# Kernel optimization log

Hardware: AMD Instinct MI355X
Metric: run time of the kernel (lower is better)

## Reference

```python
import jax, jax.numpy as jnp
import numpy as np

COUNT = 8  # hardcoded 8x8 patch grid in the original module


def setup_inputs() -> dict:
    key = jax.random.key(0)
    kx, = jax.random.split(key, 1)
    x = jax.random.normal(kx, (8, 64, 512, 512), dtype=jnp.float32)
    gamma = jnp.zeros((1,), dtype=jnp.float32)  # nn.Parameter(torch.zeros(1))
    return {"x": x, "gamma": gamma}


def reference(x, gamma):
    B, C, H, W = x.shape
    s = H // COUNT  # stride; original uses height-derived stride for both dims
    # Extract the 8x8 grid of patches without loops:
    # (B,C,H,W) -> (B,C,cnt,s,cnt,s) -> (B,cnt,cnt,C,s,s) -> (B,P,C,s*s)
    p = x.reshape(B, C, COUNT, s, COUNT, s)
    p = p.transpose(0, 2, 4, 1, 3, 5).reshape(B, COUNT * COUNT, C, s * s)
    # channel-channel energy per patch: [B,P,C,C]
    energy = jnp.einsum('bpci,bpdi->bpcd', p, p)
    # DANet trick: max - energy, then softmax over last dim
    energy_new = jnp.max(energy, axis=-1, keepdims=True) - energy
    attention = jax.nn.softmax(energy_new, axis=-1)
    out = jnp.einsum('bpcd,bpdi->bpci', attention, p)
    # reassemble spatial map
    out = out.reshape(B, COUNT, COUNT, C, s, s)
    out = out.transpose(0, 3, 1, 4, 2, 5).reshape(B, C, H, W)
    # NOTE: in the torch code y = x is an alias and x is overwritten in-place,
    # so the final result is gamma * attended + attended.
    return gamma[0] * out + out
```

## Files before the change

### kernel.cpp

```cpp
#include <hip/hip_runtime.h>


#define NC  64
#define NW  512
#define HWs 262144
#define NST 32

typedef __attribute__((ext_vector_type(8)))  __bf16 bf8;
typedef __attribute__((ext_vector_type(16))) float  f32x16;

__device__ __forceinline__ unsigned short bf16rne(float f) {
  unsigned int u = __float_as_uint(f);
  u += 0x7fffu + ((u >> 16) & 1u);
  return (unsigned short)(u >> 16);
}
__device__ __forceinline__ float fromb(unsigned short h) {
  return __uint_as_float(((unsigned int)h) << 16);
}

extern "C" __global__ __launch_bounds__(256, 4)
void spectralAgg_kernel(const float* __restrict__ x, const float* __restrict__ g,
                        float* __restrict__ out) {
  __shared__ char lds[40960];
  char* sH = lds;
  char* sL = lds + 16384;
  char* sA = lds + 32768;

  const int t   = threadIdx.x;
  const int wv  = t >> 6;
  const int l   = t & 63;
  const int l31 = l & 31;
  const int hh  = l >> 5;

  const int wg = blockIdx.x;
  const int b  = wg >> 6;
  const int pp = wg & 63;
  const int pr = pp >> 3, pc = pp & 7;
  const size_t pbase = (size_t)b * NC * HWs + (size_t)(pr * 64) * NW + (size_t)(pc * 64);
  const float* xp = x + pbase;
  float* op = out + pbase;

  const int ct = wv >> 1, dt = wv & 1;
  f32x16 accG, accS;
#pragma unroll
  for (int r = 0; r < 16; ++r) { accG[r] = 0.f; accS[r] = 0.f; }

  const char* pA  = sH + (ct * 32 + l31) * 256;
  const char* pBh = sH + (dt * 32 + l31) * 256;
  const char* pBl = sL + (dt * 32 + l31) * 256;
  const int swzH = (l & 15) << 4;

  for (int st = 0; st < NST; ++st) {
#pragma unroll 4
    for (int k = 0; k < 8; ++k) {
      const int L = t + (k << 8);
      const int c = L >> 5, q = L & 31;
      const int rl = q >> 4, col = (q & 15) << 2;
      const float4 v = *(const float4*)(xp + (size_t)c * HWs + (size_t)(st * 2 + rl) * NW + col);
      const int i0  = rl * 64 + col;
      const int off = (c << 8) + (((i0 << 1)) ^ ((c & 15) << 4));
      const unsigned short h0 = bf16rne(v.x), h1 = bf16rne(v.y),
                           h2 = bf16rne(v.z), h3 = bf16rne(v.w);
      ushort4 hv; hv.x = h0; hv.y = h1; hv.z = h2; hv.w = h3;
      *(ushort4*)(sH + off) = hv;
      ushort4 lv;
      lv.x = bf16rne(v.x - fromb(h0));
      lv.y = bf16rne(v.y - fromb(h1));
      lv.z = bf16rne(v.z - fromb(h2));
      lv.w = bf16rne(v.w - fromb(h3));
      *(ushort4*)(sL + off) = lv;
    }
    __syncthreads();
#pragma unroll
    for (int k0 = 0; k0 < 8; ++k0) {
      const int off = ((k0 << 5) + (hh << 4)) ^ swzH;
      const bf8 a  = *(const bf8*)(pA  + off);
      const bf8 bh = *(const bf8*)(pBh + off);
      const bf8 bl = *(const bf8*)(pBl + off);
      accG = __builtin_amdgcn_mfma_f32_32x32x16_bf16(a, bh, accG, 0, 0, 0);
      accS = __builtin_amdgcn_mfma_f32_32x32x16_bf16(a, bl, accS, 0, 0, 0);
    }
    __syncthreads();
  }

  float* S_lds = (float*)sL;
  float* E_lds = (float*)sH;
#pragma unroll
  for (int r = 0; r < 16; ++r) {
    const int cr = ct * 32 + (r & 3) + ((r >> 2) << 3) + (hh << 2);
    S_lds[cr * 64 + dt * 32 + l31] = accS[r];
  }
  __syncthreads();
#pragma unroll
  for (int r = 0; r < 16; ++r) {
    const int cr = ct * 32 + (r & 3) + ((r >> 2) << 3) + (hh << 2);
    const int d  = dt * 32 + l31;
    E_lds[cr * 64 + d] = accG[r] + accS[r] + S_lds[d * 64 + cr];
  }
  __syncthreads();

  const float gs = 1.0f + g[0];
#pragma unroll 1
  for (int rr = 0; rr < 16; ++rr) {
    const int c = wv * 16 + rr;
    const float e = E_lds[c * 64 + l];
    float mn = e;
#pragma unroll
    for (int o = 32; o; o >>= 1) mn = fminf(mn, __shfl_xor(mn, o));
    const float w = __expf(mn - e);
    float s = w;
#pragma unroll
    for (int o = 32; o; o >>= 1) s += __shfl_xor(s, o);
    const float a = gs * w / s;
    *(unsigned short*)(sA + c * 128 + (((l << 1)) ^ ((c & 7) << 4))) = bf16rne(a);
  }
  __syncthreads();

  char* sT = sH;
  const int irow = wv * 32 + l31;
  const char* pP  = sT + irow * 128;
  const int swzT  = (((irow & 7) ^ ((irow >> 3) & 3)) << 4);
  const char* pA0 = sA + l31 * 128;
  const char* pA1 = sA + (32 + l31) * 128;
  const int swzA  = (l31 & 7) << 4;

  for (int st = 0; st < NST; ++st) {
#pragma unroll 2
    for (int k = 0; k < 2; ++k) {
      const int L = t + (k << 8);
      const int cg = L >> 5, q = L & 31;
      const int c0 = cg << 2;
      const int rl = q >> 4, col = (q & 15) << 2;
      const int i0 = rl * 64 + col;
      const float* gp = xp + (size_t)c0 * HWs + (size_t)(st * 2 + rl) * NW + col;
      const float4 v0 = *(const float4*)(gp);
      const float4 v1 = *(const float4*)(gp + HWs);
      const float4 v2 = *(const float4*)(gp + 2 * (size_t)HWs);
      const float4 v3 = *(const float4*)(gp + 3 * (size_t)HWs);
      float vv[4][4];
      vv[0][0] = v0.x; vv[0][1] = v0.y; vv[0][2] = v0.z; vv[0][3] = v0.w;
      vv[1][0] = v1.x; vv[1][1] = v1.y; vv[1][2] = v1.z; vv[1][3] = v1.w;
      vv[2][0] = v2.x; vv[2][1] = v2.y; vv[2][2] = v2.z; vv[2][3] = v2.w;
      vv[3][0] = v3.x; vv[3][1] = v3.y; vv[3][2] = v3.z; vv[3][3] = v3.w;
#pragma unroll
      for (int ii = 0; ii < 4; ++ii) {
        const int ir = i0 + ii;
        ushort4 wq;
        wq.x = bf16rne(vv[0][ii]); wq.y = bf16rne(vv[1][ii]);
        wq.z = bf16rne(vv[2][ii]); wq.w = bf16rne(vv[3][ii]);
        *(ushort4*)(sT + ir * 128 + (((c0 << 1)) ^ ((((ir & 7) ^ ((ir >> 3) & 3))) << 4))) = wq;
      }
    }
    __syncthreads();

    f32x16 o0, o1;
#pragma unroll
    for (int r = 0; r < 16; ++r) { o0[r] = 0.f; o1[r] = 0.f; }
#pragma unroll
    for (int k0 = 0; k0 < 4; ++k0) {
      const int km = (k0 << 5) + (hh << 4);
      const bf8 pa = *(const bf8*)(pP  + (km ^ swzT));
      const bf8 a0 = *(const bf8*)(pA0 + (km ^ swzA));
      const bf8 a1 = *(const bf8*)(pA1 + (km ^ swzA));
      o0 = __builtin_amdgcn_mfma_f32_32x32x16_bf16(pa, a0, o0, 0, 0, 0);
      o1 = __builtin_amdgcn_mfma_f32_32x32x16_bf16(pa, a1, o1, 0, 0, 0);
    }

#pragma unroll
    for (int rq = 0; rq < 4; ++rq) {
      const int iloc = wv * 32 + (rq << 3) + (hh << 2);
      const int grow = st * 2 + (iloc >> 6), gcol = iloc & 63;
      float* oprow = op + (size_t)grow * NW + gcol;
      float4 q0; q0.x = o0[rq * 4 + 0]; q0.y = o0[rq * 4 + 1];
                 q0.z = o0[rq * 4 + 2]; q0.w = o0[rq * 4 + 3];
      *(float4*)(oprow + (size_t)l31 * HWs) = q0;
      float4 q1; q1.x = o1[rq * 4 + 0]; q1.y = o1[rq * 4 + 1];
                 q1.z = o1[rq * 4 + 2]; q1.w = o1[rq * 4 + 3];
      *(float4*)(oprow + (size_t)(32 + l31) * HWs) = q1;
    }
    __syncthreads();
  }
}

extern "C" void kernel_launch(void* const* d_in, const int* in_sizes, int n_in,
                              void* d_out, int out_size, void* d_ws, size_t ws_size,
                              hipStream_t stream) {
  const float* x = (const float*)d_in[0];
  const float* g = (const float*)d_in[1];
  float* o = (float*)d_out;
  spectralAgg_kernel<<<dim3(512), dim3(256), 0, stream>>>(x, g, o);
}
```

Baseline: 439.4 us.

## Register-prefetch next tile and double stage width in both GEMM phases

Both phases now process four rows per stage instead of two, which halves the number of stage iterations and barriers. Each stage's global loads are prefetched into registers one step ahead so load latency overlaps the MFMA work. The attention B-fragments are hoisted into registers once before the output loop, and hardware bf16 conversions replace the manual rounding code. LDS grows to 72KB and occupancy drops to 2 blocks per CU, with much higher register pressure from the 32 float4 prefetch buffers.

```diff
diff --git a/kernel.cpp b/kernel.cpp
--- a/kernel.cpp
+++ b/kernel.cpp
@@ -1,30 +1,75 @@
 #include <hip/hip_runtime.h>
 
 
-#define NC  64
 #define NW  512
 #define HWs 262144
-#define NST 32
+#define NS1 16
+#define NS3 16
 
 typedef __attribute__((ext_vector_type(8)))  __bf16 bf8;
+typedef __attribute__((ext_vector_type(4)))  __bf16 bf4;
 typedef __attribute__((ext_vector_type(16))) float  f32x16;
 
-__device__ __forceinline__ unsigned short bf16rne(float f) {
-  unsigned int u = __float_as_uint(f);
-  u += 0x7fffu + ((u >> 16) & 1u);
-  return (unsigned short)(u >> 16);
-}
-__device__ __forceinline__ float fromb(unsigned short h) {
-  return __uint_as_float(((unsigned int)h) << 16);
-}
-
-extern "C" __global__ __launch_bounds__(256, 4)
+#define F4C(v, k) ((k) == 0 ? (v).x : (k) == 1 ? (v).y : (k) == 2 ? (v).z : (v).w)
+
+__device__ __forceinline__ void load1(const float* g1, int st, float4 (&R)[16]) {
+  const float* gp = g1 + (size_t)st * 4 * NW;
+#pragma unroll
+  for (int rl = 0; rl < 4; ++rl)
+#pragma unroll
+    for (int j = 0; j < 4; ++j)
+      R[rl * 4 + j] = *(const float4*)(gp + (size_t)rl * NW + j * 4);
+}
+
+__device__ __forceinline__ void cvtw1(char* wH, char* wL, int q_ld, int swzw,
+                                      const float4 (&R)[16]) {
+#pragma unroll
+  for (int rl = 0; rl < 4; ++rl)
+#pragma unroll
+    for (int s = 0; s < 2; ++s) {
+      const float4 va = R[rl * 4 + s * 2], vb = R[rl * 4 + s * 2 + 1];
+      const float f[8] = {va.x, va.y, va.z, va.w, vb.x, vb.y, vb.z, vb.w};
+      bf8 h, lo;
+#pragma unroll
+      for (int e = 0; e < 8; ++e) {
+        h[e]  = (__bf16)f[e];
+        lo[e] = (__bf16)(f[e] - (float)h[e]);
+      }
+      const int boff = (rl * 128 + q_ld * 32 + s * 16) ^ swzw;
+      *(bf8*)(wH + boff) = h;
+      *(bf8*)(wL + boff) = lo;
+    }
+}
+
+__device__ __forceinline__ void load3(const float* g3, int st, float4 (&R)[16]) {
+  const float* gp = g3 + (size_t)st * 4 * NW;
+#pragma unroll
+  for (int cc = 0; cc < 4; ++cc)
+#pragma unroll
+    for (int j = 0; j < 4; ++j)
+      R[cc * 4 + j] = *(const float4*)(gp + (size_t)cc * HWs + j * 4);
+}
+
+__device__ __forceinline__ void cvtw3(char* sT, int cg, int iq, const float4 (&R)[16]) {
+#pragma unroll
+  for (int w = 0; w < 16; ++w) {
+    bf4 q;
+#pragma unroll
+    for (int cc = 0; cc < 4; ++cc)
+      q[cc] = (__bf16)F4C(R[cc * 4 + (w >> 2)], w & 3);
+    const int iloc = iq * 16 + w;
+    const int boff = (iloc & 127) * 256 + (((((iloc >> 7) << 7)) + cg * 8) ^ (w << 4));
+    *(bf4*)(sT + boff) = q;
+  }
+}
+
+extern "C" __global__ __launch_bounds__(256, 2)
 void spectralAgg_kernel(const float* __restrict__ x, const float* __restrict__ g,
                         float* __restrict__ out) {
-  __shared__ char lds[40960];
+  __shared__ char lds[73728];
   char* sH = lds;
-  char* sL = lds + 16384;
-  char* sA = lds + 32768;
+  char* sL = lds + 32768;
+  char* sA = lds + 65536;
 
   const int t   = threadIdx.x;
   const int wv  = t >> 6;
@@ -36,44 +81,36 @@
   const int b  = wg >> 6;
   const int pp = wg & 63;
   const int pr = pp >> 3, pc = pp & 7;
-  const size_t pbase = (size_t)b * NC * HWs + (size_t)(pr * 64) * NW + (size_t)(pc * 64);
+  const size_t pbase = (size_t)b * 64 * HWs + (size_t)(pr * 64) * NW + (size_t)(pc * 64);
   const float* xp = x + pbase;
   float* op = out + pbase;
 
+  const int c_ld = t >> 2, q_ld = t & 3;
+  const float* g1 = xp + (size_t)c_ld * HWs + q_ld * 16;
+  char* wH = sH + c_ld * 512;
+  char* wL = sL + c_ld * 512;
+  const int swzw = (c_ld & 31) << 4;
+
   const int ct = wv >> 1, dt = wv & 1;
+  const char* pA  = sH + (size_t)(ct * 32 + l31) * 512;
+  const char* pBh = sH + (size_t)(dt * 32 + l31) * 512;
+  const char* pBl = sL + (size_t)(dt * 32 + l31) * 512;
+  const int swzr = l31 << 4;
+
   f32x16 accG, accS;
 #pragma unroll
   for (int r = 0; r < 16; ++r) { accG[r] = 0.f; accS[r] = 0.f; }
 
-  const char* pA  = sH + (ct * 32 + l31) * 256;
-  const char* pBh = sH + (dt * 32 + l31) * 256;
-  const char* pBl = sL + (dt * 32 + l31) * 256;
-  const int swzH = (l & 15) << 4;
-
-  for (int st = 0; st < NST; ++st) {
-#pragma unroll 4
-    for (int k = 0; k < 8; ++k) {
-      const int L = t + (k << 8);
-      const int c = L >> 5, q = L & 31;
-      const int rl = q >> 4, col = (q & 15) << 2;
-      const float4 v = *(const float4*)(xp + (size_t)c * HWs + (size_t)(st * 2 + rl) * NW + col);
-      const int i0  = rl * 64 + col;
-      const int off = (c << 8) + (((i0 << 1)) ^ ((c & 15) << 4));
-      const unsigned short h0 = bf16rne(v.x), h1 = bf16rne(v.y),
-                           h2 = bf16rne(v.z), h3 = bf16rne(v.w);
-      ushort4 hv; hv.x = h0; hv.y = h1; hv.z = h2; hv.w = h3;
-      *(ushort4*)(sH + off) = hv;
-      ushort4 lv;
-      lv.x = bf16rne(v.x - fromb(h0));
-      lv.y = bf16rne(v.y - fromb(h1));
-      lv.z = bf16rne(v.z - fromb(h2));
-      lv.w = bf16rne(v.w - fromb(h3));
-      *(ushort4*)(sL + off) = lv;
-    }
-    __syncthreads();
-#pragma unroll
-    for (int k0 = 0; k0 < 8; ++k0) {
-      const int off = ((k0 << 5) + (hh << 4)) ^ swzH;
+  float4 ra[16], rb[16];
+  load1(g1, 0, ra);
+
+  for (int st = 0; st < NS1; ++st) {
+    load1(g1, (st + 1 < NS1) ? st + 1 : st, rb);
+    cvtw1(wH, wL, q_ld, swzw, ra);
+    __syncthreads();
+#pragma unroll
+    for (int k0 = 0; k0 < 16; ++k0) {
+      const int off = (k0 * 32 + hh * 16) ^ swzr;
       const bf8 a  = *(const bf8*)(pA  + off);
       const bf8 bh = *(const bf8*)(pBh + off);
       const bf8 bl = *(const bf8*)(pBl + off);
@@ -81,6 +118,8 @@
       accS = __builtin_amdgcn_mfma_f32_32x32x16_bf16(a, bl, accS, 0, 0, 0);
     }
     __syncthreads();
+#pragma unroll
+    for (int e = 0; e < 16; ++e) ra[e] = rb[e];
   }
 
   float* S_lds = (float*)sL;
@@ -98,6 +137,10 @@
     E_lds[cr * 64 + d] = accG[r] + accS[r] + S_lds[d * 64 + cr];
   }
   __syncthreads();
+
+  const int cg = t >> 4, iq = t & 15;
+  const float* g3 = xp + (size_t)(cg * 4) * HWs + (size_t)(iq >> 2) * NW + (iq & 3) * 16;
+  load3(g3, 0, ra);
 
   const float gs = 1.0f + g[0];
 #pragma unroll 1
@@ -112,73 +155,65 @@
 #pragma unroll
     for (int o = 32; o; o >>= 1) s += __shfl_xor(s, o);
     const float a = gs * w / s;
-    *(unsigned short*)(sA + c * 128 + (((l << 1)) ^ ((c & 7) << 4))) = bf16rne(a);
+    *(__bf16*)(sA + c * 128 + ((l * 2) ^ ((c & 7) << 4))) = (__bf16)a;
   }
   __syncthreads();
 
-  char* sT = sH;
-  const int irow = wv * 32 + l31;
-  const char* pP  = sT + irow * 128;
-  const int swzT  = (((irow & 7) ^ ((irow >> 3) & 3)) << 4);
-  const char* pA0 = sA + l31 * 128;
-  const char* pA1 = sA + (32 + l31) * 128;
-  const int swzA  = (l31 & 7) << 4;
-
-  for (int st = 0; st < NST; ++st) {
-#pragma unroll 2
-    for (int k = 0; k < 2; ++k) {
-      const int L = t + (k << 8);
-      const int cg = L >> 5, q = L & 31;
-      const int c0 = cg << 2;
-      const int rl = q >> 4, col = (q & 15) << 2;
-      const int i0 = rl * 64 + col;
-      const float* gp = xp + (size_t)c0 * HWs + (size_t)(st * 2 + rl) * NW + col;
-      const float4 v0 = *(const float4*)(gp);
-      const float4 v1 = *(const float4*)(gp + HWs);
-      const float4 v2 = *(const float4*)(gp + 2 * (size_t)HWs);
-      const float4 v3 = *(const float4*)(gp + 3 * (size_t)HWs);
-      float vv[4][4];
-      vv[0][0] = v0.x; vv[0][1] = v0.y; vv[0][2] = v0.z; vv[0][3] = v0.w;
-      vv[1][0] = v1.x; vv[1][1] = v1.y; vv[1][2] = v1.z; vv[1][3] = v1.w;
-      vv[2][0] = v2.x; vv[2][1] = v2.y; vv[2][2] = v2.z; vv[2][3] = v2.w;
-      vv[3][0] = v3.x; vv[3][1] = v3.y; vv[3][2] = v3.z; vv[3][3] = v3.w;
-#pragma unroll
-      for (int ii = 0; ii < 4; ++ii) {
-        const int ir = i0 + ii;
-        ushort4 wq;
-        wq.x = bf16rne(vv[0][ii]); wq.y = bf16rne(vv[1][ii]);
-        wq.z = bf16rne(vv[2][ii]); wq.w = bf16rne(vv[3][ii]);
-        *(ushort4*)(sT + ir * 128 + (((c0 << 1)) ^ ((((ir & 7) ^ ((ir >> 3) & 3))) << 4))) = wq;
+  bf8 bfr[2][4];
+#pragma unroll
+  for (int c2 = 0; c2 < 2; ++c2)
+#pragma unroll
+    for (int k0 = 0; k0 < 4; ++k0)
+      bfr[c2][k0] = *(const bf8*)(sA + (size_t)(c2 * 32 + l31) * 128 +
+                                  ((k0 * 32 + hh * 16) ^ ((l31 & 7) << 4)));
+
+  for (int st = 0; st < NS3; ++st) {
+    load3(g3, (st + 1 < NS3) ? st + 1 : st, rb);
+    cvtw3(sH, cg, iq, ra);
+    __syncthreads();
+
+    f32x16 oo[2][2];
+#pragma unroll
+    for (int it = 0; it < 2; ++it)
+#pragma unroll
+      for (int c2 = 0; c2 < 2; ++c2)
+#pragma unroll
+        for (int r = 0; r < 16; ++r) oo[it][c2][r] = 0.f;
+
+#pragma unroll
+    for (int it = 0; it < 2; ++it) {
+      const int i = wv * 64 + it * 32 + l31;
+      const char* base = sH + (size_t)(i & 127) * 256;
+      const int hb = (i >> 7) * 128;
+      const int sw = (i & 15) << 4;
+#pragma unroll
+      for (int k0 = 0; k0 < 4; ++k0) {
+        const bf8 pa = *(const bf8*)(base + ((hb + k0 * 32 + hh * 16) ^ sw));
+        oo[it][0] = __builtin_amdgcn_mfma_f32_32x32x16_bf16(pa, bfr[0][k0], oo[it][0], 0, 0, 0);
+        oo[it][1] = __builtin_amdgcn_mfma_f32_32x32x16_bf16(pa, bfr[1][k0], oo[it][1], 0, 0, 0);
       }
     }
-    __syncthreads();
-
-    f32x16 o0, o1;
-#pragma unroll
-    for (int r = 0; r < 16; ++r) { o0[r] = 0.f; o1[r] = 0.f; }
-#pragma unroll
-    for (int k0 = 0; k0 < 4; ++k0) {
-      const int km = (k0 << 5) + (hh << 4);
-      const bf8 pa = *(const bf8*)(pP  + (km ^ swzT));
-      const bf8 a0 = *(const bf8*)(pA0 + (km ^ swzA));
-      const bf8 a1 = *(const bf8*)(pA1 + (km ^ swzA));
-      o0 = __builtin_amdgcn_mfma_f32_32x32x16_bf16(pa, a0, o0, 0, 0, 0);
-      o1 = __builtin_amdgcn_mfma_f32_32x32x16_bf16(pa, a1, o1, 0, 0, 0);
-    }
-
-#pragma unroll
-    for (int rq = 0; rq < 4; ++rq) {
-      const int iloc = wv * 32 + (rq << 3) + (hh << 2);
-      const int grow = st * 2 + (iloc >> 6), gcol = iloc & 63;
-      float* oprow = op + (size_t)grow * NW + gcol;
-      float4 q0; q0.x = o0[rq * 4 + 0]; q0.y = o0[rq * 4 + 1];
-                 q0.z = o0[rq * 4 + 2]; q0.w = o0[rq * 4 + 3];
-      *(float4*)(oprow + (size_t)l31 * HWs) = q0;
-      float4 q1; q1.x = o1[rq * 4 + 0]; q1.y = o1[rq * 4 + 1];
-                 q1.z = o1[rq * 4 + 2]; q1.w = o1[rq * 4 + 3];
-      *(float4*)(oprow + (size_t)(32 + l31) * HWs) = q1;
-    }
-    __syncthreads();
+
+#pragma unroll
+    for (int it = 0; it < 2; ++it)
+#pragma unroll
+      for (int c2 = 0; c2 < 2; ++c2) {
+        const size_t cof = (size_t)(c2 * 32 + l31) * HWs;
+#pragma unroll
+        for (int rq = 0; rq < 4; ++rq) {
+          const int iloc = wv * 64 + it * 32 + rq * 8 + hh * 4;
+          const int grow = st * 4 + (iloc >> 6), gcol = iloc & 63;
+          float4 q;
+          q.x = oo[it][c2][rq * 4 + 0];
+          q.y = oo[it][c2][rq * 4 + 1];
+          q.z = oo[it][c2][rq * 4 + 2];
+          q.w = oo[it][c2][rq * 4 + 3];
+          *(float4*)(op + cof + (size_t)grow * NW + gcol) = q;
+        }
+      }
+    __syncthreads();
+#pragma unroll
+    for (int e = 0; e < 16; ++e) ra[e] = rb[e];
   }
 }
 
```

After: 388.1 us. -11.7%, faster.
